# Kernel optimization log

Hardware: AMD Instinct MI355X
Metric: run time of the kernel (lower is better)

Reference implementation:

```python
import jax, jax.numpy as jnp
import numpy as np

EPS = 1e-6  # torch.pairwise_distance default eps

def _linear(x, w, b):
    return x @ w.T + b

def _patch_attend(x, patches):
    # x: [B, C]; patches: [B, C, S]
    # torch.pairwise_distance(x.view(B,C,1), patches) -> [B, S] (norm over C)
    d = jnp.sqrt(jnp.sum((x[:, :, None] - patches + EPS) ** 2, axis=1))  # [B,S]
    p = jax.nn.softmax(jnp.exp(-d), axis=1)                              # [B,S]
    return jnp.einsum('bcs,bs->bc', patches, p)                          # [B,C]

def _get_D_and_A_m(HSI_D, LiDAR_D, data_HSI, data_LiDAR, m, K,
                   w1a, b1a, w2a, b2a):
    # Reconstructed get_D_and_A_m: cross-attention between batch features and
    # dictionary atoms using the attention net, with momentum dictionary update.
    # HSI_D, LiDAR_D: [30, D_num] (transposed dictionaries); data_*: [B, 30]
    # attention: H1 = lin1(H); D1 = lin2(D.T).T; H2 = lin1(H).T; D2 = lin2(D.T)
    H1_h = _linear(data_HSI, w1a, b1a)          # [B,60]
    D2_h = _linear(HSI_D.T, w2a, b2a)           # [D_num,60]
    S_h = H1_h @ D2_h.T                          # [B, D_num]
    A_h = jax.nn.softmax(S_h, axis=1)            # [B, D_num]
    out_h = A_h @ HSI_D.T                        # [B, 30]
    newD_h = m * HSI_D + (1.0 - m) * (data_HSI.T @ A_h)  # [30, D_num]

    H1_l = _linear(data_LiDAR, w1a, b1a)
    D2_l = _linear(LiDAR_D.T, w2a, b2a)
    S_l = H1_l @ D2_l.T
    A_l = jax.nn.softmax(S_l, axis=1)
    out_l = A_l @ LiDAR_D.T
    newD_l = m * LiDAR_D + (1.0 - m) * (data_LiDAR.T @ A_l)

    # A returned transposed ([60?]) -- model does HSI_A = HSI_A.T then cat dim=1
    # and out expects 120 features => A here must be [60, B]-like. We project
    # attended output through lin1 to get 60-dim features, transpose for return.
    feat_h = _linear(out_h, w1a, b1a).T          # [60, B]
    feat_l = _linear(out_l, w1a, b1a).T          # [60, B]
    return out_h, feat_h, newD_h, out_l, feat_l, newD_l

def setup_inputs():
    key = jax.random.key(0)
    ks = jax.random.split(key, 24)
    f = jax.random.normal
    inp = {
        'H_HSI': f(ks[0], (16384, 63), jnp.float32),
        'H_LiDAR': f(ks[1], (16384, 1), jnp.float32),
        'HSI_D': f(ks[2], (64, 63), jnp.float32),
        'LiDAR_D': f(ks[3], (64, 1), jnp.float32),
        'Patch_HSI': f(ks[4], (16384, 63, 49), jnp.float32),
        'Patch_LiDAR': f(ks[5], (16384, 1, 49), jnp.float32),
        'D_Patch_HSI': f(ks[6], (64, 63, 49), jnp.float32),
        'D_Patch_LiDAR': f(ks[7], (64, 1, 49), jnp.float32),
        'K': 10, 'm': 1, 'batchsize': 16384, 'D_num': 64,
    }
    def lin(k, o, i):
        k1, k2 = jax.random.split(k)
        s = 1.0 / np.sqrt(i)
        return (jax.random.uniform(k1, (o, i), jnp.float32, -s, s),
                jax.random.uniform(k2, (o,), jnp.float32, -s, s))
    inp['w1_1'], inp['b1_1'] = lin(ks[8], 45, 63)
    inp['w1_2'], inp['b1_2'] = lin(ks[9], 30, 45)
    inp['w2_1'], inp['b2_1'] = lin(ks[10], 15, 1)
    inp['w2_2'], inp['b2_2'] = lin(ks[11], 30, 15)
    inp['wa1'], inp['ba1'] = lin(ks[12], 60, 30)
    inp['wa2'], inp['ba2'] = lin(ks[13], 60, 30)
    inp['wo1'], inp['bo1'] = lin(ks[14], 60, 120)
    inp['wo2'], inp['bo2'] = lin(ks[15], 7, 60)
    return inp

def reference(H_HSI, H_LiDAR, HSI_D, LiDAR_D, Patch_HSI, Patch_LiDAR,
              D_Patch_HSI, D_Patch_LiDAR, K, m, batchsize, D_num,
              w1_1, b1_1, w1_2, b1_2, w2_1, b2_1, w2_2, b2_2,
              wa1, ba1, wa2, ba2, wo1, bo1, wo2, bo2):
    # patch attention aggregation for each branch
    SP_HSI = _patch_attend(H_HSI.reshape(H_HSI.shape[0], -1), Patch_HSI)
    SP_LiDAR = _patch_attend(H_LiDAR.reshape(H_LiDAR.shape[0], -1), Patch_LiDAR)
    D_SP_HSI = _patch_attend(HSI_D.reshape(HSI_D.shape[0], -1), D_Patch_HSI)
    D_SP_LiDAR = _patch_attend(LiDAR_D.reshape(LiDAR_D.shape[0], -1), D_Patch_LiDAR)

    lin1 = lambda x: _linear(_linear(x, w1_1, b1_1), w1_2, b1_2)  # 63->30
    lin2 = lambda x: _linear(_linear(x, w2_1, b2_1), w2_2, b2_2)  # 1->30

    data_HSI = lin1(SP_HSI)          # [B,30]
    data_LiDAR = lin2(SP_LiDAR)      # [B,30]
    HSI_Dp = lin1(D_SP_HSI).T        # [30,D_num]
    LiDAR_Dp = lin2(D_SP_LiDAR).T    # [30,D_num]

    mf = jnp.float32(m)
    out_h, HSI_A, HSI_Dn, out_l, LiDAR_A, LiDAR_Dn = _get_D_and_A_m(
        HSI_Dp, LiDAR_Dp, data_HSI, data_LiDAR, mf, K, wa1, ba1, wa2, ba2)

    HSI_A = HSI_A.T      # [B,60]
    LiDAR_A = LiDAR_A.T  # [B,60]
    A = jnp.concatenate([LiDAR_A, HSI_A], axis=1)  # [B,120]
    output = _linear(_linear(A, wo1, bo1), wo2, bo2)  # [B,Classes]
    return (data_HSI, data_LiDAR, HSI_A, HSI_Dn, LiDAR_A, LiDAR_Dn, output)
```

## Files before the change

kernel.cpp:

```cpp
#include <hip/hip_runtime.h>
#include <math.h>

#define NB 16384
#define DN 64
#define ST 68
#define OFF1 491520
#define OFF2 983040
#define OFF3 1966080
#define OFF4 1968000
#define OFF5 2951040
#define OFF6 2952960
#define SPH_OFF  0
#define SPL_OFF  1032192
#define DSPH_OFF 1048576
#define DSPL_OFF 1052608
#define DPTH_OFF 1052672
#define DPTL_OFF 1054592
#define D2H_OFF  1056512
#define D2L_OFF  1060352
#define AH_OFF   1064192
#define AL_OFF   2112768
#define PH_OFF   3161344
#define PL_OFF   3284224

typedef const __attribute__((address_space(1))) void* gas_ptr;
typedef __attribute__((address_space(3))) void* las_ptr;

__device__ __forceinline__ float wredmax(float v) {
#pragma unroll
    for (int m = 32; m; m >>= 1) v = fmaxf(v, __shfl_xor(v, m, 64));
    return v;
}
__device__ __forceinline__ float wredsum(float v) {
#pragma unroll
    for (int m = 32; m; m >>= 1) v += __shfl_xor(v, m, 64);
    return v;
}

template<int CH>
__device__ __forceinline__ void load_chunk(const float* __restrict__ xrow, float* __restrict__ x) {
    const int NQ = CH >> 2;
#pragma unroll
    for (int q = 0; q < NQ; ++q) {
        float4 v = *(const float4*)(xrow + 4 * q);
        x[4 * q] = v.x; x[4 * q + 1] = v.y; x[4 * q + 2] = v.z; x[4 * q + 3] = v.w;
    }
#pragma unroll
    for (int j = NQ * 4; j < CH; ++j) x[j] = xrow[j];
}

template<int INS, int RS, int PER>
__device__ __forceinline__ void dlayer4(const float* __restrict__ W,
                                        const float* __restrict__ bias,
                                        const float* __restrict__ xb,
                                        float* __restrict__ yb,
                                        const int OUTS, const int o0,
                                        const float scale)
{
    float acc[PER];
#pragma unroll
    for (int k = 0; k < PER; ++k) {
        int oc = o0 + k; oc = oc < OUTS ? oc : OUTS - 1;
        acc[k] = bias ? bias[oc] : 0.0f;
    }
#pragma unroll
    for (int c0 = 0; c0 < INS; c0 += 16) {
        constexpr int REM = 0;  (void)REM;
        const int CHv = (INS - c0) < 16 ? (INS - c0) : 16;
        float x[16];
        if (CHv == 16) load_chunk<16>(xb + c0, x);
        else if (CHv == 15) load_chunk<15>(xb + c0, x);
        else if (CHv == 14) load_chunk<14>(xb + c0, x);
        else if (CHv == 13) load_chunk<13>(xb + c0, x);
        else if (CHv == 12) load_chunk<12>(xb + c0, x);
        else {
#pragma unroll
            for (int j = 0; j < 16; ++j) if (j < CHv) x[j] = xb[c0 + j];
        }
#pragma unroll
        for (int k = 0; k < PER; ++k) {
            int oc = o0 + k; oc = oc < OUTS ? oc : OUTS - 1;
            const float* Wr = W + oc * RS + c0;
            float a = acc[k];
#pragma unroll
            for (int j = 0; j < 16; ++j) if (j < CHv) a = fmaf(Wr[j], x[j], a);
            acc[k] = a;
        }
    }
#pragma unroll
    for (int k = 0; k < PER; ++k) {
        int o = o0 + k;
        if (o < OUTS) yb[o] = acc[k] * scale;
    }
}

template<int INS, int CS, int PER>
__device__ __forceinline__ void dlayerT4(const float* __restrict__ W,
                                         const float* __restrict__ xb,
                                         float* __restrict__ yb,
                                         const int OUTS, const int o0,
                                         const float scale)
{
    float acc[PER];
#pragma unroll
    for (int k = 0; k < PER; ++k) acc[k] = 0.0f;
#pragma unroll
    for (int c0 = 0; c0 < INS; c0 += 16) {
        float x[16];
        load_chunk<16>(xb + c0, x);
#pragma unroll
        for (int j = 0; j < 16; ++j) {
            const float* Wr = W + (c0 + j) * CS + o0;
#pragma unroll
            for (int k = 0; k < PER; ++k) acc[k] = fmaf(Wr[k], x[j], acc[k]);
        }
    }
#pragma unroll
    for (int k = 0; k < PER; ++k) {
        int o = o0 + k;
        if (o < OUTS) yb[o] = acc[k] * scale;
    }
}

__device__ __forceinline__ void softmax_exp4(const float* __restrict__ Sb,
                                             float* __restrict__ Qb,
                                             float* __restrict__ P,
                                             const int w, const int l)
{
    const float4* S4 = (const float4*)Sb;
    float4 m4 = S4[0];
#pragma unroll
    for (int q = 1; q < 16; ++q) {
        float4 v = S4[q];
        m4.x = fmaxf(m4.x, v.x); m4.y = fmaxf(m4.y, v.y);
        m4.z = fmaxf(m4.z, v.z); m4.w = fmaxf(m4.w, v.w);
    }
    const float mx = fmaxf(fmaxf(m4.x, m4.y), fmaxf(m4.z, m4.w));
    float4 sv = S4[w];
    float4 e;
    e.x = __expf(sv.x - mx); e.y = __expf(sv.y - mx);
    e.z = __expf(sv.z - mx); e.w = __expf(sv.w - mx);
    ((float4*)Qb)[w] = e;
    P[w * 64 + l] = (e.x + e.y) + (e.z + e.w);
}

__device__ __forceinline__ float inv16(const float* __restrict__ P, const int l)
{
    float s0 = P[l], s1 = P[64 + l], s2 = P[128 + l], s3 = P[192 + l];
#pragma unroll
    for (int g = 4; g < 16; g += 4) {
        s0 += P[g * 64 + l];
        s1 += P[(g + 1) * 64 + l];
        s2 += P[(g + 2) * 64 + l];
        s3 += P[(g + 3) * 64 + l];
    }
    return 1.0f / ((s0 + s1) + (s2 + s3));
}

template<int INS, int RS, int PER>
__device__ __forceinline__ void dlayer(const float* __restrict__ W,
                                       const float* __restrict__ bias,
                                       const float* __restrict__ xb,
                                       float* __restrict__ yb,
                                       const int OUTS, const int o0,
                                       const float scale)
{
    float acc[PER];
#pragma unroll
    for (int k = 0; k < PER; ++k) {
        int oc = o0 + k; oc = oc < OUTS ? oc : OUTS - 1;
        acc[k] = bias ? bias[oc] : 0.0f;
    }
#pragma unroll
    for (int c0 = 0; c0 < INS; c0 += 16) {
        const int CH = (INS - c0) < 16 ? (INS - c0) : 16;
        float x[16];
#pragma unroll
        for (int j = 0; j < CH; ++j) x[j] = xb[c0 + j];
#pragma unroll
        for (int k = 0; k < PER; ++k) {
            int oc = o0 + k; oc = oc < OUTS ? oc : OUTS - 1;
            const float* Wr = W + oc * RS + c0;
            float a = acc[k];
#pragma unroll
            for (int j = 0; j < CH; ++j) a = fmaf(Wr[j], x[j], a);
            acc[k] = a;
        }
    }
#pragma unroll
    for (int k = 0; k < PER; ++k) {
        int o = o0 + k;
        if (o < OUTS) yb[o] = acc[k] * scale;
    }
}

__global__ __launch_bounds__(256) void patch_attend_kernel(
    const float* __restrict__ patchH, const float* __restrict__ xH,
    const float* __restrict__ patchL, const float* __restrict__ xL,
    float* __restrict__ spH, float* __restrict__ spL,
    const float* __restrict__ dpH, const float* __restrict__ dxH,
    const float* __restrict__ dpL, const float* __restrict__ dxL,
    float* __restrict__ dspH, float* __restrict__ dspL)
{
    __shared__ __align__(16) float ph[4 * 3087];
    __shared__ __align__(16) float pl_[4 * 49];
    __shared__ __align__(16) float xh[4 * 63];
    __shared__ float xls[4];
    __shared__ float pw[4 * 49];

    const int tid = threadIdx.x;
    const bool isD = blockIdx.x >= (NB / 4);
    const int b0 = (isD ? (blockIdx.x - NB / 4) : blockIdx.x) * 4;
    const float* PH = isD ? dpH : patchH;
    const float* XH = isD ? dxH : xH;
    const float* PL = isD ? dpL : patchL;
    const float* XL = isD ? dxL : xL;
    float* SH = isD ? dspH : spH;
    float* SL = isD ? dspL : spL;
    {
        const float4* s4 = (const float4*)(PH + (size_t)b0 * 3087);
        float4* d4 = (float4*)ph;
        for (int i = tid; i < 3087; i += 256) {
            __builtin_amdgcn_global_load_lds((gas_ptr)(const void*)(s4 + i),
                                             (las_ptr)(void*)(d4 + i), 16, 0, 0);
        }
        if (tid < 49) ((float4*)pl_)[tid] = ((const float4*)(PL + (size_t)b0 * 49))[tid];
        if (tid >= 64 && tid < 127) ((float4*)xh)[tid - 64] = ((const float4*)(XH + (size_t)b0 * 63))[tid - 64];
        if (tid == 255) *((float4*)xls) = *((const float4*)(XL + b0));
    }
    asm volatile("s_waitcnt vmcnt(0)" ::: "memory");
    __syncthreads();

    const int w = tid >> 6, l = tid & 63;
    const float* phw = ph + w * 3087;
    const float* plw = pl_ + w * 49;
    const float* xhw = xh + w * 63;
    const float xlw = xls[w];

    float eh = -INFINITY, el = -INFINITY;
    if (l < 49) {
        float acc = 0.f;
#pragma unroll
        for (int c = 0; c < 63; ++c) {
            float t = xhw[c] - phw[c * 49 + l] + 1e-6f;
            acc = fmaf(t, t, acc);
        }
        eh = __expf(-sqrtf(acc));
        float tl = xlw - plw[l] + 1e-6f;
        el = __expf(-fabsf(tl));
    }
    float mh = wredmax(eh), ml = wredmax(el);
    float qh = (l < 49) ? __expf(eh - mh) : 0.f;
    float ql = (l < 49) ? __expf(el - ml) : 0.f;
    float sh = wredsum(qh);
    float sl = wredsum(ql);
    if (l < 49) pw[w * 49 + l] = qh / sh;
    float spl_v = wredsum((l < 49) ? plw[l] * (ql / sl) : 0.f);
    if (l == 0) SL[b0 + w] = spl_v;
    __syncthreads();
    if (l < 63) {
        float acc = 0.f;
        const float* pww = pw + w * 49;
#pragma unroll
        for (int s = 0; s < 49; ++s) acc = fmaf(phw[l * 49 + s], pww[s], acc);
        SH[(size_t)(b0 + w) * 63 + l] = acc;
    }
}

__global__ __launch_bounds__(1024) void dict_chain_kernel(
    const float* __restrict__ dsph, const float* __restrict__ dspl,
    const float* __restrict__ w1_1, const float* __restrict__ b1_1,
    const float* __restrict__ w1_2, const float* __restrict__ b1_2,
    const float* __restrict__ w2_1, const float* __restrict__ b2_1,
    const float* __restrict__ w2_2, const float* __restrict__ b2_2,
    const float* __restrict__ wa2, const float* __restrict__ ba2,
    float* __restrict__ dptH, float* __restrict__ dptL,
    float* __restrict__ d2H, float* __restrict__ d2L)
{
    __shared__ float B0[64 * 65];
    __shared__ float B1[64 * 65];
    __shared__ float XLs[64];
    const int tid = threadIdx.x;
    const int w = __builtin_amdgcn_readfirstlane(tid >> 6);
    const int l = tid & 63;
    {
        const float4* s4 = (const float4*)dsph;
        float4* d4 = (float4*)B0;
        if (tid < 1008) d4[tid] = s4[tid];
        else if (tid >= 1008 && tid < 1024 && (tid - 1008) < 16)
            ((float4*)XLs)[tid - 1008] = ((const float4*)dspl)[tid - 1008];
    }
    __syncthreads();
    dlayer<63, 63, 3>(w1_1, b1_1, B0 + l * 63, B1 + l * 45, 45, w * 3, 1.0f);
    __syncthreads();
    dlayer<45, 45, 2>(w1_2, b1_2, B1 + l * 45, B0 + l * 30, 30, w * 2, 1.0f);
    __syncthreads();
    for (int i = tid; i < 1920; i += 1024) dptH[i] = B0[i];
    dlayer<30, 30, 4>(wa2, ba2, B0 + l * 30, B1 + l * 61, 60, w * 4, 1.0f);
    __syncthreads();
    for (int i = tid; i < 3840; i += 1024) { int r = i / 60, c = i - r * 60; d2H[i] = B1[r * 61 + c]; }
    dlayer<1, 1, 1>(w2_1, b2_1, XLs + l, B0 + l * 15, 15, w, 1.0f);
    __syncthreads();
    dlayer<15, 15, 2>(w2_2, b2_2, B0 + l * 15, B1 + l * 30, 30, w * 2, 1.0f);
    __syncthreads();
    for (int i = tid; i < 1920; i += 1024) dptL[i] = B1[i];
    dlayer<30, 30, 4>(wa2, ba2, B1 + l * 30, B0 + l * 61, 60, w * 4, 1.0f);
    __syncthreads();
    for (int i = tid; i < 3840; i += 1024) { int r = i / 60, c = i - r * 60; d2L[i] = B0[r * 61 + c]; }
}

__global__ __launch_bounds__(1024) void chain_kernel(
    const float* __restrict__ spH, const float* __restrict__ spL,
    const float* __restrict__ dptH, const float* __restrict__ dptL,
    const float* __restrict__ d2H, const float* __restrict__ d2L,
    const float* __restrict__ w1_1, const float* __restrict__ b1_1,
    const float* __restrict__ w1_2, const float* __restrict__ b1_2,
    const float* __restrict__ w2_1, const float* __restrict__ b2_1,
    const float* __restrict__ w2_2, const float* __restrict__ b2_2,
    const float* __restrict__ wa1, const float* __restrict__ ba1,
    const float* __restrict__ wo1, const float* __restrict__ bo1,
    const float* __restrict__ wo2, const float* __restrict__ bo2,
    const int* __restrict__ mI,
    float* __restrict__ out, float* __restrict__ aH, float* __restrict__ aL)
{
    __shared__ __align__(16) float HA[64 * ST];
    __shared__ __align__(16) float HB[64 * ST];
    __shared__ __align__(16) float LA[64 * ST];
    __shared__ __align__(16) float LB[64 * ST];
    __shared__ float XLs[64];
    __shared__ float PH[16 * 64], PL[16 * 64];

    const int tid = threadIdx.x;
    const int w = __builtin_amdgcn_readfirstlane(tid >> 6);
    const int l = tid & 63;
    const int b0 = blockIdx.x * 64;
    const int b = b0 + l;
    const float mf = (float)(*mI);

    for (int i = tid; i < 4032; i += 1024) {
        int r = i / 63, c = i - r * 63;
        HA[r * ST + c] = spH[(size_t)b0 * 63 + i];
    }
    if (tid < 64) XLs[tid] = spL[b0 + tid];
    __syncthreads();

    dlayer4<63, 63, 3>(w1_1, b1_1, HA + l * ST, HB + l * ST, 45, w * 3, 1.0f);
    dlayer4<1, 1, 1>(w2_1, b2_1, XLs + l, LA + l * ST, 15, w, 1.0f);
    __syncthreads();
    dlayer4<45, 45, 2>(w1_2, b1_2, HB + l * ST, HA + l * ST, 30, w * 2, 1.0f);
    dlayer4<15, 15, 2>(w2_2, b2_2, LA + l * ST, LB + l * ST, 30, w * 2, 1.0f);
    __syncthreads();
    for (int i = tid; i < 1920; i += 1024) {
        int r = i / 30, c = i - r * 30;
        out[(size_t)b0 * 30 + i] = HA[r * ST + c];
        out[OFF1 + (size_t)b0 * 30 + i] = LB[r * ST + c];
    }
    dlayer4<30, 30, 4>(wa1, ba1, HA + l * ST, HB + l * ST, 60, w * 4, 1.0f);
    dlayer4<30, 30, 4>(wa1, ba1, LB + l * ST, LA + l * ST, 60, w * 4, 1.0f);
    __syncthreads();
    dlayer4<60, 60, 4>(d2H, nullptr, HB + l * ST, HA + l * ST, 64, w * 4, 1.0f);
    dlayer4<60, 60, 4>(d2L, nullptr, LA + l * ST, LB + l * ST, 64, w * 4, 1.0f);
    __syncthreads();
    softmax_exp4(HA + l * ST, HB + l * ST, PH, w, l);
    softmax_exp4(LB + l * ST, LA + l * ST, PL, w, l);
    __syncthreads();
    if (mf != 1.0f) {
        for (int i = tid; i < 4096; i += 1024) {
            int r = i >> 6, j = i & 63;
            aH[(size_t)b0 * 64 + i] = HB[r * ST + j] * inv16(PH, r);
            aL[(size_t)b0 * 64 + i] = LA[r * ST + j] * inv16(PL, r);
        }
    }
    {
        const float invH = inv16(PH, l);
        const float invL = inv16(PL, l);
        dlayerT4<64, 30, 2>(dptH, HB + l * ST, HA + l * ST, 30, w * 2, invH);
        dlayerT4<64, 30, 2>(dptL, LA + l * ST, LB + l * ST, 30, w * 2, invL);
    }
    __syncthreads();
    dlayer4<30, 30, 4>(wa1, ba1, HA + l * ST, HB + l * ST, 60, w * 4, 1.0f);
    dlayer4<30, 30, 4>(wa1, ba1, LB + l * ST, LA + l * ST, 60, w * 4, 1.0f);
    __syncthreads();
    for (int i = tid; i < 3840; i += 1024) {
        int r = i / 60, c = i - r * 60;
        out[OFF2 + (size_t)b0 * 60 + i] = HB[r * ST + c];
        out[OFF4 + (size_t)b0 * 60 + i] = LA[r * ST + c];
    }
    {
        const int o0 = w * 4;
        float acc[4];
#pragma unroll
        for (int k = 0; k < 4; ++k) acc[k] = (o0 + k < 60) ? bo1[o0 + k] : 0.0f;
#pragma unroll
        for (int c0 = 0; c0 < 60; c0 += 16) {
            const int CH = (60 - c0) < 16 ? (60 - c0) : 16;
            float x[16];
            if (CH == 16) load_chunk<16>(LA + l * ST + c0, x);
            else load_chunk<12>(LA + l * ST + c0, x);
#pragma unroll
            for (int k = 0; k < 4; ++k) {
                int oc = o0 + k; oc = oc < 60 ? oc : 59;
                const float* Wr = wo1 + oc * 120 + c0;
                float a = acc[k];
#pragma unroll
                for (int j = 0; j < 16; ++j) if (j < CH) a = fmaf(Wr[j], x[j], a);
                acc[k] = a;
            }
        }
#pragma unroll
        for (int c0 = 0; c0 < 60; c0 += 16) {
            const int CH = (60 - c0) < 16 ? (60 - c0) : 16;
            float x[16];
            if (CH == 16) load_chunk<16>(HB + l * ST + c0, x);
            else load_chunk<12>(HB + l * ST + c0, x);
#pragma unroll
            for (int k = 0; k < 4; ++k) {
                int oc = o0 + k; oc = oc < 60 ? oc : 59;
                const float* Wr = wo1 + oc * 120 + 60 + c0;
                float a = acc[k];
#pragma unroll
                for (int j = 0; j < 16; ++j) if (j < CH) a = fmaf(Wr[j], x[j], a);
                acc[k] = a;
            }
        }
        float4 av; av.x = acc[0]; av.y = acc[1]; av.z = acc[2]; av.w = acc[3];
        *((float4*)(HA + l * ST + o0)) = av;
    }
    __syncthreads();
    if (w < 7) {
        float a = bo2[w];
        const float* Wr = wo2 + w * 60;
#pragma unroll
        for (int c0 = 0; c0 < 60; c0 += 16) {
            const int CH = (60 - c0) < 16 ? (60 - c0) : 16;
            float x[16];
            if (CH == 16) load_chunk<16>(HA + l * ST + c0, x);
            else load_chunk<12>(HA + l * ST + c0, x);
#pragma unroll
            for (int j = 0; j < 16; ++j) if (j < CH) a = fmaf(Wr[c0 + j], x[j], a);
        }
        out[OFF6 + (size_t)b * 7 + w] = a;
    }
}

__global__ __launch_bounds__(256) void momentum_partial_kernel(
    const float* __restrict__ dataH, const float* __restrict__ dataL,
    const float* __restrict__ aH, const float* __restrict__ aL,
    float* __restrict__ pH, float* __restrict__ pL,
    const int* __restrict__ mI)
{
    const float mf = (float)(*mI);
    if (mf == 1.0f) return;
    const int tid = threadIdx.x;
    const int chunk = blockIdx.x & 63;
    const int mod = blockIdx.x >> 6;
    const float* data = mod ? dataL : dataH;
    const float* A = mod ? aL : aH;
    float* P = mod ? pL : pH;
    const int b0 = chunk * 256;
    const int j = tid & 63;
    const int g = tid >> 6;
    float acc[8];
#pragma unroll
    for (int k = 0; k < 8; ++k) acc[k] = 0.f;
    for (int bb = 0; bb < 256; ++bb) {
        float a = A[(size_t)(b0 + bb) * 64 + j];
#pragma unroll
        for (int k = 0; k < 8; ++k) {
            int c = g + 4 * k; c = c < 30 ? c : 29;
            acc[k] = fmaf(data[(size_t)(b0 + bb) * 30 + c], a, acc[k]);
        }
    }
#pragma unroll
    for (int k = 0; k < 8; ++k) {
        int c = g + 4 * k;
        if (c < 30) P[chunk * 1920 + c * 64 + j] = acc[k];
    }
}

__global__ __launch_bounds__(256) void momentum_final_kernel(
    const float* __restrict__ dptH, const float* __restrict__ dptL,
    const float* __restrict__ pH, const float* __restrict__ pL,
    const int* __restrict__ mI, float* __restrict__ out)
{
    int t = blockIdx.x * 256 + threadIdx.x;
    if (t >= 3840) return;
    const int mod = t >= 1920;
    const int idx = mod ? t - 1920 : t;
    const int c = idx >> 6, j = idx & 63;
    const float mf = (float)(*mI);
    const float* dpt = mod ? dptL : dptH;
    float v = mf * dpt[j * 30 + c];
    if (mf != 1.0f) {
        const float* P = mod ? pL : pH;
        float s = 0.f;
        for (int k = 0; k < 64; ++k) s += P[k * 1920 + idx];
        v += (1.0f - mf) * s;
    }
    out[(mod ? OFF5 : OFF3) + idx] = v;
}

extern "C" void kernel_launch(void* const* d_in, const int* in_sizes, int n_in,
                              void* d_out, int out_size, void* d_ws, size_t ws_size,
                              hipStream_t stream) {
    const float* H_HSI        = (const float*)d_in[0];
    const float* H_LiDAR      = (const float*)d_in[1];
    const float* HSI_D        = (const float*)d_in[2];
    const float* LiDAR_D      = (const float*)d_in[3];
    const float* Patch_HSI    = (const float*)d_in[4];
    const float* Patch_LiDAR  = (const float*)d_in[5];
    const float* D_Patch_HSI  = (const float*)d_in[6];
    const float* D_Patch_LiDAR= (const float*)d_in[7];
    const int*   mI           = (const int*)d_in[9];
    const float* w1_1 = (const float*)d_in[12];
    const float* b1_1 = (const float*)d_in[13];
    const float* w1_2 = (const float*)d_in[14];
    const float* b1_2 = (const float*)d_in[15];
    const float* w2_1 = (const float*)d_in[16];
    const float* b2_1 = (const float*)d_in[17];
    const float* w2_2 = (const float*)d_in[18];
    const float* b2_2 = (const float*)d_in[19];
    const float* wa1  = (const float*)d_in[20];
    const float* ba1  = (const float*)d_in[21];
    const float* wa2  = (const float*)d_in[22];
    const float* ba2  = (const float*)d_in[23];
    const float* wo1  = (const float*)d_in[24];
    const float* bo1  = (const float*)d_in[25];
    const float* wo2  = (const float*)d_in[26];
    const float* bo2  = (const float*)d_in[27];

    float* out = (float*)d_out;
    float* ws  = (float*)d_ws;

    patch_attend_kernel<<<NB / 4 + DN / 4, 256, 0, stream>>>(
        Patch_HSI, H_HSI, Patch_LiDAR, H_LiDAR, ws + SPH_OFF, ws + SPL_OFF,
        D_Patch_HSI, HSI_D, D_Patch_LiDAR, LiDAR_D, ws + DSPH_OFF, ws + DSPL_OFF);
    dict_chain_kernel<<<1, 1024, 0, stream>>>(
        ws + DSPH_OFF, ws + DSPL_OFF,
        w1_1, b1_1, w1_2, b1_2, w2_1, b2_1, w2_2, b2_2, wa2, ba2,
        ws + DPTH_OFF, ws + DPTL_OFF, ws + D2H_OFF, ws + D2L_OFF);
    chain_kernel<<<NB / 64, 1024, 0, stream>>>(
        ws + SPH_OFF, ws + SPL_OFF,
        ws + DPTH_OFF, ws + DPTL_OFF, ws + D2H_OFF, ws + D2L_OFF,
        w1_1, b1_1, w1_2, b1_2, w2_1, b2_1, w2_2, b2_2,
        wa1, ba1, wo1, bo1, wo2, bo2, mI,
        out, ws + AH_OFF, ws + AL_OFF);
    momentum_partial_kernel<<<128, 256, 0, stream>>>(
        out, out + OFF1, ws + AH_OFF, ws + AL_OFF, ws + PH_OFF, ws + PL_OFF, mI);
    momentum_final_kernel<<<15, 256, 0, stream>>>(
        ws + DPTH_OFF, ws + DPTL_OFF, ws + PH_OFF, ws + PL_OFF, mI, out);
}
```

Baseline: 87.13 us.

## Split waves between HSI and LiDAR branches, pad rows, fold momentum via atomics

The chain kernels now give half the waves to the HSI branch and half to the LiDAR branch, each wave computing more outputs, instead of every wave running both branches in turn. The patch-attend output rows are padded to 64 floats so tiles load with aligned float4 reads. The momentum reduction drops its final kernel: dict_chain writes m*D directly and partial sums are atomically added into the output. This cuts one launch and serialized per-wave work, at the cost of atomic contention and a non-deterministic summation order.

```diff
diff --git a/kernel.cpp b/kernel.cpp
--- a/kernel.cpp
+++ b/kernel.cpp
@@ -11,17 +11,15 @@
 #define OFF5 2951040
 #define OFF6 2952960
 #define SPH_OFF  0
-#define SPL_OFF  1032192
-#define DSPH_OFF 1048576
-#define DSPL_OFF 1052608
-#define DPTH_OFF 1052672
-#define DPTL_OFF 1054592
-#define D2H_OFF  1056512
-#define D2L_OFF  1060352
-#define AH_OFF   1064192
-#define AL_OFF   2112768
-#define PH_OFF   3161344
-#define PL_OFF   3284224
+#define SPL_OFF  1048576
+#define DSPH_OFF 1064960
+#define DSPL_OFF 1069056
+#define DPTH_OFF 1069120
+#define DPTL_OFF 1071040
+#define D2H_OFF  1072960
+#define D2L_OFF  1076800
+#define AH_OFF   1080640
+#define AL_OFF   2129216
 
 typedef const __attribute__((address_space(1))) void* gas_ptr;
 typedef __attribute__((address_space(3))) void* las_ptr;
@@ -65,7 +63,6 @@
     }
 #pragma unroll
     for (int c0 = 0; c0 < INS; c0 += 16) {
-        constexpr int REM = 0;  (void)REM;
         const int CHv = (INS - c0) < 16 ? (INS - c0) : 16;
         float x[16];
         if (CHv == 16) load_chunk<16>(xb + c0, x);
@@ -122,10 +119,10 @@
     }
 }
 
-__device__ __forceinline__ void softmax_exp4(const float* __restrict__ Sb,
+__device__ __forceinline__ void softmax_exp8(const float* __restrict__ Sb,
                                              float* __restrict__ Qb,
                                              float* __restrict__ P,
-                                             const int w, const int l)
+                                             const int wb, const int l)
 {
     const float4* S4 = (const float4*)Sb;
     float4 m4 = S4[0];
@@ -136,62 +133,22 @@
         m4.z = fmaxf(m4.z, v.z); m4.w = fmaxf(m4.w, v.w);
     }
     const float mx = fmaxf(fmaxf(m4.x, m4.y), fmaxf(m4.z, m4.w));
-    float4 sv = S4[w];
-    float4 e;
-    e.x = __expf(sv.x - mx); e.y = __expf(sv.y - mx);
-    e.z = __expf(sv.z - mx); e.w = __expf(sv.w - mx);
-    ((float4*)Qb)[w] = e;
-    P[w * 64 + l] = (e.x + e.y) + (e.z + e.w);
-}
-
-__device__ __forceinline__ float inv16(const float* __restrict__ P, const int l)
-{
-    float s0 = P[l], s1 = P[64 + l], s2 = P[128 + l], s3 = P[192 + l];
-#pragma unroll
-    for (int g = 4; g < 16; g += 4) {
-        s0 += P[g * 64 + l];
-        s1 += P[(g + 1) * 64 + l];
-        s2 += P[(g + 2) * 64 + l];
-        s3 += P[(g + 3) * 64 + l];
-    }
+    float4 a = S4[2 * wb], bq = S4[2 * wb + 1];
+    float4 ea, eb;
+    ea.x = __expf(a.x - mx); ea.y = __expf(a.y - mx);
+    ea.z = __expf(a.z - mx); ea.w = __expf(a.w - mx);
+    eb.x = __expf(bq.x - mx); eb.y = __expf(bq.y - mx);
+    eb.z = __expf(bq.z - mx); eb.w = __expf(bq.w - mx);
+    ((float4*)Qb)[2 * wb] = ea;
+    ((float4*)Qb)[2 * wb + 1] = eb;
+    P[wb * 64 + l] = ((ea.x + ea.y) + (ea.z + ea.w)) + ((eb.x + eb.y) + (eb.z + eb.w));
+}
+
+__device__ __forceinline__ float inv8(const float* __restrict__ P, const int l)
+{
+    float s0 = P[l] + P[64 + l], s1 = P[128 + l] + P[192 + l];
+    float s2 = P[256 + l] + P[320 + l], s3 = P[384 + l] + P[448 + l];
     return 1.0f / ((s0 + s1) + (s2 + s3));
-}
-
-template<int INS, int RS, int PER>
-__device__ __forceinline__ void dlayer(const float* __restrict__ W,
-                                       const float* __restrict__ bias,
-                                       const float* __restrict__ xb,
-                                       float* __restrict__ yb,
-                                       const int OUTS, const int o0,
-                                       const float scale)
-{
-    float acc[PER];
-#pragma unroll
-    for (int k = 0; k < PER; ++k) {
-        int oc = o0 + k; oc = oc < OUTS ? oc : OUTS - 1;
-        acc[k] = bias ? bias[oc] : 0.0f;
-    }
-#pragma unroll
-    for (int c0 = 0; c0 < INS; c0 += 16) {
-        const int CH = (INS - c0) < 16 ? (INS - c0) : 16;
-        float x[16];
-#pragma unroll
-        for (int j = 0; j < CH; ++j) x[j] = xb[c0 + j];
-#pragma unroll
-        for (int k = 0; k < PER; ++k) {
-            int oc = o0 + k; oc = oc < OUTS ? oc : OUTS - 1;
-            const float* Wr = W + oc * RS + c0;
-            float a = acc[k];
-#pragma unroll
-            for (int j = 0; j < CH; ++j) a = fmaf(Wr[j], x[j], a);
-            acc[k] = a;
-        }
-    }
-#pragma unroll
-    for (int k = 0; k < PER; ++k) {
-        int o = o0 + k;
-        if (o < OUTS) yb[o] = acc[k] * scale;
-    }
 }
 
 __global__ __launch_bounds__(256) void patch_attend_kernel(
@@ -263,7 +220,7 @@
         const float* pww = pw + w * 49;
 #pragma unroll
         for (int s = 0; s < 49; ++s) acc = fmaf(phw[l * 49 + s], pww[s], acc);
-        SH[(size_t)(b0 + w) * 63 + l] = acc;
+        SH[(size_t)(b0 + w) * 64 + l] = acc;
     }
 }
 
@@ -275,38 +232,58 @@
     const float* __restrict__ w2_2, const float* __restrict__ b2_2,
     const float* __restrict__ wa2, const float* __restrict__ ba2,
     float* __restrict__ dptH, float* __restrict__ dptL,
-    float* __restrict__ d2H, float* __restrict__ d2L)
-{
-    __shared__ float B0[64 * 65];
-    __shared__ float B1[64 * 65];
+    float* __restrict__ d2H, float* __restrict__ d2L,
+    const int* __restrict__ mI, float* __restrict__ out)
+{
+    __shared__ __align__(16) float HA[64 * ST];
+    __shared__ __align__(16) float HB[64 * ST];
+    __shared__ __align__(16) float LA[64 * ST];
+    __shared__ __align__(16) float LB[64 * ST];
     __shared__ float XLs[64];
     const int tid = threadIdx.x;
     const int w = __builtin_amdgcn_readfirstlane(tid >> 6);
+    const int wb = w & 7;
+    const bool isH = w < 8;
     const int l = tid & 63;
+    const float mf = (float)(*mI);
     {
-        const float4* s4 = (const float4*)dsph;
-        float4* d4 = (float4*)B0;
-        if (tid < 1008) d4[tid] = s4[tid];
-        else if (tid >= 1008 && tid < 1024 && (tid - 1008) < 16)
-            ((float4*)XLs)[tid - 1008] = ((const float4*)dspl)[tid - 1008];
-    }
-    __syncthreads();
-    dlayer<63, 63, 3>(w1_1, b1_1, B0 + l * 63, B1 + l * 45, 45, w * 3, 1.0f);
-    __syncthreads();
-    dlayer<45, 45, 2>(w1_2, b1_2, B1 + l * 45, B0 + l * 30, 30, w * 2, 1.0f);
-    __syncthreads();
-    for (int i = tid; i < 1920; i += 1024) dptH[i] = B0[i];
-    dlayer<30, 30, 4>(wa2, ba2, B0 + l * 30, B1 + l * 61, 60, w * 4, 1.0f);
-    __syncthreads();
-    for (int i = tid; i < 3840; i += 1024) { int r = i / 60, c = i - r * 60; d2H[i] = B1[r * 61 + c]; }
-    dlayer<1, 1, 1>(w2_1, b2_1, XLs + l, B0 + l * 15, 15, w, 1.0f);
-    __syncthreads();
-    dlayer<15, 15, 2>(w2_2, b2_2, B0 + l * 15, B1 + l * 30, 30, w * 2, 1.0f);
-    __syncthreads();
-    for (int i = tid; i < 1920; i += 1024) dptL[i] = B1[i];
-    dlayer<30, 30, 4>(wa2, ba2, B1 + l * 30, B0 + l * 61, 60, w * 4, 1.0f);
-    __syncthreads();
-    for (int i = tid; i < 3840; i += 1024) { int r = i / 60, c = i - r * 60; d2L[i] = B0[r * 61 + c]; }
+        int r = tid >> 4, q = tid & 15;
+        *(float4*)(HA + r * ST + 4 * q) = ((const float4*)dsph)[tid];
+        if (tid < 64) XLs[tid] = dspl[tid];
+    }
+    __syncthreads();
+    if (isH) {
+        dlayer4<63, 63, 6>(w1_1, b1_1, HA + l * ST, HB + l * ST, 45, wb * 6, 1.0f);
+    } else {
+        const float xl = XLs[l];
+#pragma unroll
+        for (int k = 0; k < 2; ++k) {
+            int o = wb * 2 + k;
+            if (o < 15) LB[l * ST + o] = fmaf(w2_1[o], xl, b2_1[o]);
+        }
+    }
+    __syncthreads();
+    if (isH) dlayer4<45, 45, 4>(w1_2, b1_2, HB + l * ST, HA + l * ST, 30, wb * 4, 1.0f);
+    else     dlayer4<15, 15, 4>(w2_2, b2_2, LB + l * ST, LA + l * ST, 30, wb * 4, 1.0f);
+    __syncthreads();
+    for (int i = tid; i < 1920; i += 1024) {
+        int r = i / 30, c = i - r * 30;
+        dptH[i] = HA[r * ST + c];
+        dptL[i] = LA[r * ST + c];
+    }
+    for (int i = tid; i < 1920; i += 1024) {
+        int c = i >> 6, j = i & 63;
+        out[OFF3 + i] = mf * HA[j * ST + c];
+        out[OFF5 + i] = mf * LA[j * ST + c];
+    }
+    if (isH) dlayer4<30, 30, 8>(wa2, ba2, HA + l * ST, HB + l * ST, 60, wb * 8, 1.0f);
+    else     dlayer4<30, 30, 8>(wa2, ba2, LA + l * ST, LB + l * ST, 60, wb * 8, 1.0f);
+    __syncthreads();
+    for (int i = tid; i < 3840; i += 1024) {
+        int r = i / 60, c = i - r * 60;
+        d2H[i] = HB[r * ST + c];
+        d2L[i] = LB[r * ST + c];
+    }
 }
 
 __global__ __launch_bounds__(1024) void chain_kernel(
@@ -328,63 +305,74 @@
     __shared__ __align__(16) float LA[64 * ST];
     __shared__ __align__(16) float LB[64 * ST];
     __shared__ float XLs[64];
-    __shared__ float PH[16 * 64], PL[16 * 64];
+    __shared__ float PH[8 * 64], PL[8 * 64];
 
     const int tid = threadIdx.x;
     const int w = __builtin_amdgcn_readfirstlane(tid >> 6);
+    const int wb = w & 7;
+    const bool isH = w < 8;
     const int l = tid & 63;
     const int b0 = blockIdx.x * 64;
     const int b = b0 + l;
     const float mf = (float)(*mI);
 
-    for (int i = tid; i < 4032; i += 1024) {
-        int r = i / 63, c = i - r * 63;
-        HA[r * ST + c] = spH[(size_t)b0 * 63 + i];
-    }
-    if (tid < 64) XLs[tid] = spL[b0 + tid];
-    __syncthreads();
-
-    dlayer4<63, 63, 3>(w1_1, b1_1, HA + l * ST, HB + l * ST, 45, w * 3, 1.0f);
-    dlayer4<1, 1, 1>(w2_1, b2_1, XLs + l, LA + l * ST, 15, w, 1.0f);
-    __syncthreads();
-    dlayer4<45, 45, 2>(w1_2, b1_2, HB + l * ST, HA + l * ST, 30, w * 2, 1.0f);
-    dlayer4<15, 15, 2>(w2_2, b2_2, LA + l * ST, LB + l * ST, 30, w * 2, 1.0f);
+    {
+        int r = tid >> 4, q = tid & 15;
+        *(float4*)(HA + r * ST + 4 * q) = ((const float4*)(spH + (size_t)b0 * 64))[tid];
+        if (tid < 64) XLs[tid] = spL[b0 + tid];
+    }
+    __syncthreads();
+    if (isH) {
+        dlayer4<63, 63, 6>(w1_1, b1_1, HA + l * ST, HB + l * ST, 45, wb * 6, 1.0f);
+    } else {
+        const float xl = XLs[l];
+#pragma unroll
+        for (int k = 0; k < 2; ++k) {
+            int o = wb * 2 + k;
+            if (o < 15) LB[l * ST + o] = fmaf(w2_1[o], xl, b2_1[o]);
+        }
+    }
+    __syncthreads();
+    if (isH) dlayer4<45, 45, 4>(w1_2, b1_2, HB + l * ST, HA + l * ST, 30, wb * 4, 1.0f);
+    else     dlayer4<15, 15, 4>(w2_2, b2_2, LB + l * ST, LA + l * ST, 30, wb * 4, 1.0f);
     __syncthreads();
     for (int i = tid; i < 1920; i += 1024) {
         int r = i / 30, c = i - r * 30;
         out[(size_t)b0 * 30 + i] = HA[r * ST + c];
-        out[OFF1 + (size_t)b0 * 30 + i] = LB[r * ST + c];
-    }
-    dlayer4<30, 30, 4>(wa1, ba1, HA + l * ST, HB + l * ST, 60, w * 4, 1.0f);
-    dlayer4<30, 30, 4>(wa1, ba1, LB + l * ST, LA + l * ST, 60, w * 4, 1.0f);
-    __syncthreads();
-    dlayer4<60, 60, 4>(d2H, nullptr, HB + l * ST, HA + l * ST, 64, w * 4, 1.0f);
-    dlayer4<60, 60, 4>(d2L, nullptr, LA + l * ST, LB + l * ST, 64, w * 4, 1.0f);
-    __syncthreads();
-    softmax_exp4(HA + l * ST, HB + l * ST, PH, w, l);
-    softmax_exp4(LB + l * ST, LA + l * ST, PL, w, l);
+        out[OFF1 + (size_t)b0 * 30 + i] = LA[r * ST + c];
+    }
+    if (isH) dlayer4<30, 30, 8>(wa1, ba1, HA + l * ST, HB + l * ST, 60, wb * 8, 1.0f);
+    else     dlayer4<30, 30, 8>(wa1, ba1, LA + l * ST, LB + l * ST, 60, wb * 8, 1.0f);
+    __syncthreads();
+    if (isH) dlayer4<60, 60, 8>(d2H, nullptr, HB + l * ST, HA + l * ST, 64, wb * 8, 1.0f);
+    else     dlayer4<60, 60, 8>(d2L, nullptr, LB + l * ST, LA + l * ST, 64, wb * 8, 1.0f);
+    __syncthreads();
+    if (isH) softmax_exp8(HA + l * ST, HB + l * ST, PH, wb, l);
+    else     softmax_exp8(LA + l * ST, LB + l * ST, PL, wb, l);
     __syncthreads();
     if (mf != 1.0f) {
-        for (int i = tid; i < 4096; i += 1024) {
-            int r = i >> 6, j = i & 63;
-            aH[(size_t)b0 * 64 + i] = HB[r * ST + j] * inv16(PH, r);
-            aL[(size_t)b0 * 64 + i] = LA[r * ST + j] * inv16(PL, r);
-        }
-    }
-    {
-        const float invH = inv16(PH, l);
-        const float invL = inv16(PL, l);
-        dlayerT4<64, 30, 2>(dptH, HB + l * ST, HA + l * ST, 30, w * 2, invH);
-        dlayerT4<64, 30, 2>(dptL, LA + l * ST, LB + l * ST, 30, w * 2, invL);
-    }
-    __syncthreads();
-    dlayer4<30, 30, 4>(wa1, ba1, HA + l * ST, HB + l * ST, 60, w * 4, 1.0f);
-    dlayer4<30, 30, 4>(wa1, ba1, LB + l * ST, LA + l * ST, 60, w * 4, 1.0f);
+        if (isH) {
+            for (int i = tid; i < 4096; i += 512) {
+                int r = i >> 6, j = i & 63;
+                aH[(size_t)b0 * 64 + i] = HB[r * ST + j] * inv8(PH, r);
+            }
+        } else {
+            for (int i = tid - 512; i < 4096; i += 512) {
+                int r = i >> 6, j = i & 63;
+                aL[(size_t)b0 * 64 + i] = LB[r * ST + j] * inv8(PL, r);
+            }
+        }
+    }
+    if (isH) dlayerT4<64, 30, 4>(dptH, HB + l * ST, HA + l * ST, 30, wb * 4, inv8(PH, l));
+    else     dlayerT4<64, 30, 4>(dptL, LB + l * ST, LA + l * ST, 30, wb * 4, inv8(PL, l));
+    __syncthreads();
+    if (isH) dlayer4<30, 30, 8>(wa1, ba1, HA + l * ST, HB + l * ST, 60, wb * 8, 1.0f);
+    else     dlayer4<30, 30, 8>(wa1, ba1, LA + l * ST, LB + l * ST, 60, wb * 8, 1.0f);
     __syncthreads();
     for (int i = tid; i < 3840; i += 1024) {
         int r = i / 60, c = i - r * 60;
         out[OFF2 + (size_t)b0 * 60 + i] = HB[r * ST + c];
-        out[OFF4 + (size_t)b0 * 60 + i] = LA[r * ST + c];
+        out[OFF4 + (size_t)b0 * 60 + i] = LB[r * ST + c];
     }
     {
         const int o0 = w * 4;
@@ -395,8 +383,8 @@
         for (int c0 = 0; c0 < 60; c0 += 16) {
             const int CH = (60 - c0) < 16 ? (60 - c0) : 16;
             float x[16];
-            if (CH == 16) load_chunk<16>(LA + l * ST + c0, x);
-            else load_chunk<12>(LA + l * ST + c0, x);
+            if (CH == 16) load_chunk<16>(LB + l * ST + c0, x);
+            else load_chunk<12>(LB + l * ST + c0, x);
 #pragma unroll
             for (int k = 0; k < 4; ++k) {
                 int oc = o0 + k; oc = oc < 60 ? oc : 59;
@@ -423,8 +411,10 @@
                 acc[k] = a;
             }
         }
-        float4 av; av.x = acc[0]; av.y = acc[1]; av.z = acc[2]; av.w = acc[3];
-        *((float4*)(HA + l * ST + o0)) = av;
+        if (o0 < 60) {
+            float4 av; av.x = acc[0]; av.y = acc[1]; av.z = acc[2]; av.w = acc[3];
+            *((float4*)(HA + l * ST + o0)) = av;
+        }
     }
     __syncthreads();
     if (w < 7) {
@@ -443,11 +433,10 @@
     }
 }
 
-__global__ __launch_bounds__(256) void momentum_partial_kernel(
+__global__ __launch_bounds__(256) void momentum_kernel(
     const float* __restrict__ dataH, const float* __restrict__ dataL,
     const float* __restrict__ aH, const float* __restrict__ aL,
-    float* __restrict__ pH, float* __restrict__ pL,
-    const int* __restrict__ mI)
+    const int* __restrict__ mI, float* __restrict__ out)
 {
     const float mf = (float)(*mI);
     if (mf == 1.0f) return;
@@ -456,7 +445,7 @@
     const int mod = blockIdx.x >> 6;
     const float* data = mod ? dataL : dataH;
     const float* A = mod ? aL : aH;
-    float* P = mod ? pL : pH;
+    float* D = out + (mod ? OFF5 : OFF3);
     const int b0 = chunk * 256;
     const int j = tid & 63;
     const int g = tid >> 6;
@@ -471,33 +460,12 @@
             acc[k] = fmaf(data[(size_t)(b0 + bb) * 30 + c], a, acc[k]);
         }
     }
+    const float s = 1.0f - mf;
 #pragma unroll
     for (int k = 0; k < 8; ++k) {
         int c = g + 4 * k;
-        if (c < 30) P[chunk * 1920 + c * 64 + j] = acc[k];
-    }
-}
-
-__global__ __launch_bounds__(256) void momentum_final_kernel(
-    const float* __restrict__ dptH, const float* __restrict__ dptL,
-    const float* __restrict__ pH, const float* __restrict__ pL,
-    const int* __restrict__ mI, float* __restrict__ out)
-{
-    int t = blockIdx.x * 256 + threadIdx.x;
-    if (t >= 3840) return;
-    const int mod = t >= 1920;
-    const int idx = mod ? t - 1920 : t;
-    const int c = idx >> 6, j = idx & 63;
-    const float mf = (float)(*mI);
-    const float* dpt = mod ? dptL : dptH;
-    float v = mf * dpt[j * 30 + c];
-    if (mf != 1.0f) {
-        const float* P = mod ? pL : pH;
-        float s = 0.f;
-        for (int k = 0; k < 64; ++k) s += P[k * 1920 + idx];
-        v += (1.0f - mf) * s;
-    }
-    out[(mod ? OFF5 : OFF3) + idx] = v;
+        if (c < 30) atomicAdd(&D[c * 64 + j], s * acc[k]);
+    }
 }
 
 extern "C" void kernel_launch(void* const* d_in, const int* in_sizes, int n_in,
@@ -538,15 +506,13 @@
     dict_chain_kernel<<<1, 1024, 0, stream>>>(
         ws + DSPH_OFF, ws + DSPL_OFF,
         w1_1, b1_1, w1_2, b1_2, w2_1, b2_1, w2_2, b2_2, wa2, ba2,
-        ws + DPTH_OFF, ws + DPTL_OFF, ws + D2H_OFF, ws + D2L_OFF);
+        ws + DPTH_OFF, ws + DPTL_OFF, ws + D2H_OFF, ws + D2L_OFF, mI, out);
     chain_kernel<<<NB / 64, 1024, 0, stream>>>(
         ws + SPH_OFF, ws + SPL_OFF,
         ws + DPTH_OFF, ws + DPTL_OFF, ws + D2H_OFF, ws + D2L_OFF,
         w1_1, b1_1, w1_2, b1_2, w2_1, b2_1, w2_2, b2_2,
         wa1, ba1, wo1, bo1, wo2, bo2, mI,
         out, ws + AH_OFF, ws + AL_OFF);
-    momentum_partial_kernel<<<128, 256, 0, stream>>>(
-        out, out + OFF1, ws + AH_OFF, ws + AL_OFF, ws + PH_OFF, ws + PL_OFF, mI);
-    momentum_final_kernel<<<15, 256, 0, stream>>>(
-        ws + DPTH_OFF, ws + DPTL_OFF, ws + PH_OFF, ws + PL_OFF, mI, out);
-}
+    momentum_kernel<<<128, 256, 0, stream>>>(
+        out, out + OFF1, ws + AH_OFF, ws + AL_OFF, mI, out);
+}
```

New measurement: 99.10 us. +13.7%, slower.
